# Kernel tuning notes

Hardware: AMD Instinct MI355X
Metric: run time of the kernel (lower is better)

The kernel has to match this reference:

```python
import jax, jax.numpy as jnp
import numpy as np

N_NODES = 100000
N_EDGES = 3200000
D_FEAT = 256
TOP_K = 50000


def setup_inputs() -> dict:
    key = jax.random.key(0)
    k1, k2, k3 = jax.random.split(key, 3)
    h = jax.random.normal(k1, (N_NODES, D_FEAT), dtype=jnp.float32)
    W = jax.random.normal(k2, (D_FEAT, 1), dtype=jnp.float32) * (1.0 / np.sqrt(D_FEAT))
    b = jnp.zeros((1,), dtype=jnp.float32)
    edge_index = jax.random.randint(k3, (2, N_EDGES), 0, N_NODES, dtype=jnp.int64)
    return {"h": h, "W": W, "b": b, "edge_index": edge_index, "top_k": TOP_K}


def reference(h, W, b, edge_index, top_k):
    # scores = sigmoid(Linear(h)) -> [N, 1]
    scores = jax.nn.sigmoid(h @ W + b)  # [N, 1]
    # top-k node selection by score (descending), like dgl.topk_nodes
    top_scores, node_ids = jax.lax.top_k(scores[:, 0], top_k)  # [k], [k]
    # gather features of selected nodes, scale by their scores
    new_h = h[node_ids] * top_scores[:, None]  # [k, d]
    # induced-subgraph edges: edge kept iff both endpoints selected
    member = jnp.zeros((h.shape[0],), dtype=bool).at[node_ids].set(True)
    edge_mask = member[edge_index[0]] & member[edge_index[1]]  # [E]
    return new_h, node_ids, edge_mask
```

## Files before the change

### kernel.cpp

```cpp
#include <hip/hip_runtime.h>
#include <math.h>

#define N_NODES 100000
#define D_FEAT  256
#define TOP_K   50000
#define NBINS   65536
#define NCHUNK  64
#define CUTPOS  (N_NODES - TOP_K)
#define ROWSTRIDE 260
#define NBITW   3200
#define FUSE_GRID   2048
#define EMIT_BLOCKS 1408


__device__ __forceinline__ int bucket_of(float s) {
    int b = (int)(s * 65536.0f);
    return min(max(b, 0), NBINS - 1);
}

__device__ __forceinline__ float np_expf(float x) {
    float q  = rintf(x * 1.44269504088896341f);
    float xr = fmaf(-q, 0.693359375f, x);
    xr       = fmaf(-q, -2.12194440e-4f, xr);
    float x2 = xr * xr;
    float p  = 1.9875691500E-4f;
    p = fmaf(p, xr, 1.3981999507E-3f);
    p = fmaf(p, xr, 8.3334519073E-3f);
    p = fmaf(p, xr, 4.1665795894E-2f);
    p = fmaf(p, xr, 1.6666665459E-1f);
    p = fmaf(p, xr, 5.0000001201E-1f);
    p = fmaf(p, x2, xr);
    p = p + 1.0f;
    return ldexpf(p, (int)q);
}

__global__ void score_kernel(const float* __restrict__ h,
                             const float* __restrict__ W,
                             const float* __restrict__ bvec,
                             float* __restrict__ s32,
                             int* __restrict__ hist) {
    __shared__ float rows[32 * ROWSTRIDE];
    __shared__ float wl[256];
    int tid  = threadIdx.x;
    int wave = tid >> 6;
    int lane = tid & 63;
    int g    = lane >> 3;
    int l    = lane & 7;

    wl[tid] = W[tid];

    int nodeBase = blockIdx.x * 32 + wave * 8;
#pragma unroll
    for (int r = 0; r < 8; ++r) {
        float4 v = ((const float4*)(h + (size_t)(nodeBase + r) * D_FEAT))[lane];
        *((float4*)&rows[(wave * 8 + r) * ROWSTRIDE + lane * 4]) = v;
    }
    __syncthreads();

    float wreg[32];
#pragma unroll
    for (int i = 0; i < 32; ++i) wreg[i] = wl[i * 8 + l];

    const float* myrow = &rows[(wave * 8 + g) * ROWSTRIDE];
    float acc = 0.0f;
#pragma unroll
    for (int i = 0; i < 32; ++i)
        acc = fmaf(myrow[i * 8 + l], wreg[i], acc);

    float b01 = acc + __shfl_xor(acc, 1, 64);
    float b23 = b01 + __shfl_xor(b01, 2, 64);
    float z   = b23 + __shfl_xor(b23, 4, 64);

    z = z + bvec[0];
    float t = np_expf(-z);
    float s = 1.0f / (1.0f + t);

    if (l == 0) {
        int node = nodeBase + g;
        s32[node] = s;
        atomicAdd(&hist[bucket_of(s)], 1);
    }
}

__global__ void scan_chunks_kernel(const int* __restrict__ hist,
                                   int* __restrict__ offs,
                                   int* __restrict__ cursor,
                                   int* __restrict__ chunkSum) {
    __shared__ int wsum[4];
    int tid  = threadIdx.x;
    int lane = tid & 63;
    int wid  = tid >> 6;
    int base = blockIdx.x * 1024 + tid * 4;

    int4 hv = *((const int4*)(hist + base));
    int e1 = hv.x;
    int e2 = hv.x + hv.y;
    int e3 = e2 + hv.z;
    int tot = e3 + hv.w;

    int incl = tot;
#pragma unroll
    for (int d = 1; d < 64; d <<= 1) {
        int t = __shfl_up(incl, d, 64);
        if (lane >= d) incl += t;
    }
    if (lane == 63) wsum[wid] = incl;
    __syncthreads();
    int wbase = 0;
#pragma unroll
    for (int w = 0; w < 3; ++w)
        if (w < wid) wbase += wsum[w];

    int excl = wbase + (incl - tot);
    int4 ov = make_int4(excl, excl + e1, excl + e2, excl + e3);
    *((int4*)(offs + base))   = ov;
    *((int4*)(cursor + base)) = ov;
    if (tid == 255) chunkSum[blockIdx.x] = excl + tot;
}

__device__ __forceinline__ void build_base(const int* __restrict__ chunkSum,
                                           int* sbase, int tid) {
    if (tid < 64) {
        int v = chunkSum[tid];
        int inc = v;
#pragma unroll
        for (int d = 1; d < 64; d <<= 1) {
            int t = __shfl_up(inc, d, 64);
            if (tid >= d) inc += t;
        }
        sbase[tid] = inc - v;
    }
}

__global__ void scatter_kernel(const float* __restrict__ s32,
                               int* __restrict__ cursor,
                               const int* __restrict__ offs,
                               const int* __restrict__ chunkSum,
                               unsigned int* __restrict__ bits,
                               float* __restrict__ ss,
                               int* __restrict__ si) {
    __shared__ int sbase[64];
    int tid = threadIdx.x;
    build_base(chunkSum, sbase, tid);
    __syncthreads();
    int i = blockIdx.x * 256 + tid;
    if (i >= N_NODES) return;
    float s = s32[i];
    int b = bucket_of(s);
    int bn = b + 1;
    int gend = (bn == NBINS) ? N_NODES : sbase[bn >> 10] + offs[bn];
    if (gend <= CUTPOS) return;
    int pos = atomicAdd(&cursor[b], 1);
    int gbase = sbase[b >> 10];
    ss[gbase + pos] = s;
    si[gbase + pos] = i;
    if (gbase + offs[b] >= CUTPOS)
        atomicOr(&bits[(unsigned)i >> 5], 1u << (i & 31));
}

__global__ void bucket_sort_kernel(const int* __restrict__ offs,
                                   const int* __restrict__ chunkSum,
                                   unsigned int* __restrict__ bits,
                                   float* __restrict__ ss,
                                   int* __restrict__ si) {
    __shared__ int sbase[64];
    int tid = threadIdx.x;
    build_base(chunkSum, sbase, tid);
    __syncthreads();
    int b = blockIdx.x * 256 + tid;
    int s0 = sbase[b >> 10] + offs[b];
    int e  = (b == NBINS - 1) ? N_NODES : sbase[(b + 1) >> 10] + offs[b + 1];
    if (e <= CUTPOS) return;
    for (int i = s0 + 1; i < e; ++i) {
        float ks = ss[i];
        int   ki = si[i];
        int j = i - 1;
        while (j >= s0) {
            float ps = ss[j];
            int   pi = si[j];
            bool gt = (ps > ks) || (ps == ks && pi < ki);
            if (!gt) break;
            ss[j + 1] = ps;
            si[j + 1] = pi;
            --j;
        }
        ss[j + 1] = ks;
        si[j + 1] = ki;
    }
    if (s0 < CUTPOS) {
        for (int i = CUTPOS; i < e; ++i) {
            int id = si[i];
            atomicOr(&bits[(unsigned)id >> 5], 1u << (id & 31));
        }
    }
}

__device__ __forceinline__ unsigned mem_bit(const unsigned int* __restrict__ bits,
                                            int s) {
    return (bits[(unsigned)s >> 5] >> (s & 31)) & 1u;
}

__global__ void emit_edge_kernel(const float* __restrict__ h,
                                 const float* __restrict__ ss,
                                 const int* __restrict__ si,
                                 const int* __restrict__ ei,
                                 const unsigned int* __restrict__ bits,
                                 float* __restrict__ out_newh,
                                 float* __restrict__ out_ids,
                                 float* __restrict__ out_mask,
                                 int E) {
    int tid = threadIdx.x;
    int bid = blockIdx.x;

    if (bid < EMIT_BLOCKS) {
        int lane = tid & 63;
        int wg   = bid * 4 + (tid >> 6);
        for (int row = wg; row < TOP_K; row += EMIT_BLOCKS * 4) {
            int p = N_NODES - 1 - row;
            int id  = si[p];
            float s = ss[p];
            if (lane == 0) out_ids[row] = (float)id;
            const float4* hv = (const float4*)(h + (size_t)id * D_FEAT);
            float4 v = hv[lane];
            ((float4*)(out_newh + (size_t)row * D_FEAT))[lane] =
                make_float4(v.x * s, v.y * s, v.z * s, v.w * s);
        }
        return;
    }

    __shared__ int sflag;
    if (tid < 64) {
        int v = ei[2 * tid + 1];
        unsigned long long m = __ballot(v == 0);
        if (tid == 0) sflag = (m == ~0ULL) ? 1 : 0;
    }
    __syncthreads();
    int flag = sflag;

    int npairs = (E + 1) / 2;
    int stride = (FUSE_GRID - EMIT_BLOCKS) * 256;
    for (int k = (bid - EMIT_BLOCKS) * 256 + tid; k < npairs; k += stride) {
        int i0 = 2 * k;
        int i1 = i0 + 1;
        if (i1 < E) {
            int s0, d0, s1, d1;
            if (flag) {
                int4 a  = ((const int4*)ei)[k];
                int4 bq = ((const int4*)(ei + 2 * (size_t)E))[k];
                s0 = a.x;  s1 = a.z;
                d0 = bq.x; d1 = bq.z;
            } else {
                int2 a  = ((const int2*)ei)[k];
                int2 bq = ((const int2*)(ei + (size_t)E))[k];
                s0 = a.x;  s1 = a.y;
                d0 = bq.x; d1 = bq.y;
            }
            bool ok0 = ((unsigned)s0 < (unsigned)N_NODES) &&
                       ((unsigned)d0 < (unsigned)N_NODES) &&
                       mem_bit(bits, s0) && mem_bit(bits, d0);
            bool ok1 = ((unsigned)s1 < (unsigned)N_NODES) &&
                       ((unsigned)d1 < (unsigned)N_NODES) &&
                       mem_bit(bits, s1) && mem_bit(bits, d1);
            ((float2*)out_mask)[k] = make_float2(ok0 ? 1.0f : 0.0f,
                                                 ok1 ? 1.0f : 0.0f);
        } else {
            int s0, d0;
            if (flag) { s0 = ei[2 * i0]; d0 = ei[2 * ((size_t)E + i0)]; }
            else      { s0 = ei[i0];     d0 = ei[(size_t)E + i0]; }
            bool ok0 = ((unsigned)s0 < (unsigned)N_NODES) &&
                       ((unsigned)d0 < (unsigned)N_NODES) &&
                       mem_bit(bits, s0) && mem_bit(bits, d0);
            out_mask[i0] = ok0 ? 1.0f : 0.0f;
        }
    }
}

extern "C" void kernel_launch(void* const* d_in, const int* in_sizes, int n_in,
                              void* d_out, int out_size, void* d_ws, size_t ws_size,
                              hipStream_t stream) {
    const float* h  = (const float*)d_in[0];
    const float* W  = (const float*)d_in[1];
    const float* bv = (const float*)d_in[2];
    const int*   ei = (const int*)d_in[3];
    const int E = in_sizes[3] / 2;

    char* ws = (char*)d_ws;
    float*        s32      = (float*)(ws + 0);
    float*        ss       = (float*)(ws + 400000);
    int*          si       = (int*)(ws + 800000);
    int*          hist     = (int*)(ws + 1200000);
    unsigned int* bits     = (unsigned int*)(ws + 1462144);
    int*          offs     = (int*)(ws + 1562144);
    int*          cursor   = (int*)(ws + 1824288);
    int*          chunkSum = (int*)(ws + 2086432);

    float* out      = (float*)d_out;
    float* out_newh = out;
    float* out_ids  = out + (size_t)TOP_K * D_FEAT;
    float* out_mask = out + (size_t)TOP_K * D_FEAT + TOP_K;

    hipMemsetAsync(ws + 1200000, 0, 274944, stream);

    score_kernel<<<N_NODES / 32, 256, 0, stream>>>(h, W, bv, s32, hist);
    scan_chunks_kernel<<<NCHUNK, 256, 0, stream>>>(hist, offs, cursor, chunkSum);
    scatter_kernel<<<(N_NODES + 255) / 256, 256, 0, stream>>>(s32, cursor, offs,
                                                              chunkSum, bits, ss, si);
    bucket_sort_kernel<<<NBINS / 256, 256, 0, stream>>>(offs, chunkSum, bits, ss, si);
    emit_edge_kernel<<<FUSE_GRID, 256, 0, stream>>>(h, ss, si, ei, bits,
                                                    out_newh, out_ids, out_mask, E);
}
```

Baseline: 238.7 us.

## Replace static block split with atomic work queue interleaving gather and edge chunks

The fused emit/edge kernel used to split blocks statically, with 1408 blocks doing row gathers and the rest doing edge-mask work. Now every block pulls chunks from a global atomic counter, and gather and edge chunks are interleaved 2:1 when the sizes match. Each gather chunk covers 8 rows and each edge chunk 512 pairs. The aim is to balance load between the two memory-bound phases and avoid tail imbalance, at the cost of one atomic plus two barriers per chunk and a slightly larger memset for the queue counter.

```diff
diff --git a/kernel.cpp b/kernel.cpp
--- a/kernel.cpp
+++ b/kernel.cpp
@@ -9,8 +9,9 @@
 #define CUTPOS  (N_NODES - TOP_K)
 #define ROWSTRIDE 260
 #define NBITW   3200
-#define FUSE_GRID   2048
-#define EMIT_BLOCKS 1408
+#define QGRID   2048
+#define EMIT_CHUNKS 6250
+#define EDGE_CHUNK_SHIFT 9
 
 
 __device__ __forceinline__ int bucket_of(float s) {
@@ -205,73 +206,104 @@
                                  const int* __restrict__ si,
                                  const int* __restrict__ ei,
                                  const unsigned int* __restrict__ bits,
+                                 int* __restrict__ queue,
                                  float* __restrict__ out_newh,
                                  float* __restrict__ out_ids,
                                  float* __restrict__ out_mask,
                                  int E) {
-    int tid = threadIdx.x;
-    int bid = blockIdx.x;
-
-    if (bid < EMIT_BLOCKS) {
-        int lane = tid & 63;
-        int wg   = bid * 4 + (tid >> 6);
-        for (int row = wg; row < TOP_K; row += EMIT_BLOCKS * 4) {
-            int p = N_NODES - 1 - row;
-            int id  = si[p];
-            float s = ss[p];
-            if (lane == 0) out_ids[row] = (float)id;
-            const float4* hv = (const float4*)(h + (size_t)id * D_FEAT);
-            float4 v = hv[lane];
-            ((float4*)(out_newh + (size_t)row * D_FEAT))[lane] =
-                make_float4(v.x * s, v.y * s, v.z * s, v.w * s);
-        }
-        return;
-    }
-
     __shared__ int sflag;
+    __shared__ int snext;
+    int tid  = threadIdx.x;
+    int lane = tid & 63;
+    int wv   = tid >> 6;
+
     if (tid < 64) {
         int v = ei[2 * tid + 1];
         unsigned long long m = __ballot(v == 0);
         if (tid == 0) sflag = (m == ~0ULL) ? 1 : 0;
     }
+
+    int npairs = (E + 1) / 2;
+    int nEdgeChunks = (npairs + ((1 << EDGE_CHUNK_SHIFT) - 1)) >> EDGE_CHUNK_SHIFT;
+    int total = EMIT_CHUNKS + nEdgeChunks;
+    bool interleave = (nEdgeChunks * 2 == EMIT_CHUNKS);
+
+    if (tid == 0) snext = atomicAdd(queue, 1);
     __syncthreads();
     int flag = sflag;
-
-    int npairs = (E + 1) / 2;
-    int stride = (FUSE_GRID - EMIT_BLOCKS) * 256;
-    for (int k = (bid - EMIT_BLOCKS) * 256 + tid; k < npairs; k += stride) {
-        int i0 = 2 * k;
-        int i1 = i0 + 1;
-        if (i1 < E) {
-            int s0, d0, s1, d1;
-            if (flag) {
-                int4 a  = ((const int4*)ei)[k];
-                int4 bq = ((const int4*)(ei + 2 * (size_t)E))[k];
-                s0 = a.x;  s1 = a.z;
-                d0 = bq.x; d1 = bq.z;
-            } else {
-                int2 a  = ((const int2*)ei)[k];
-                int2 bq = ((const int2*)(ei + (size_t)E))[k];
-                s0 = a.x;  s1 = a.y;
-                d0 = bq.x; d1 = bq.y;
+    int c = snext;
+
+    while (c < total) {
+        int grabbed = 0;
+        if (tid == 0) grabbed = atomicAdd(queue, 1);
+
+        int eIdx = -1, gIdx = -1;
+        if (interleave) {
+            int t = c / 3, r = c - 3 * t;
+            if (r < 2) eIdx = 2 * t + r; else gIdx = t;
+        } else {
+            if (c < EMIT_CHUNKS) eIdx = c; else gIdx = c - EMIT_CHUNKS;
+        }
+
+        if (eIdx >= 0) {
+            int rowBase = eIdx * 8 + wv * 2;
+#pragma unroll
+            for (int r = 0; r < 2; ++r) {
+                int row = rowBase + r;
+                int p = N_NODES - 1 - row;
+                int id  = si[p];
+                float s = ss[p];
+                if (lane == 0) out_ids[row] = (float)id;
+                const float4* hv = (const float4*)(h + (size_t)id * D_FEAT);
+                float4 v = hv[lane];
+                ((float4*)(out_newh + (size_t)row * D_FEAT))[lane] =
+                    make_float4(v.x * s, v.y * s, v.z * s, v.w * s);
             }
-            bool ok0 = ((unsigned)s0 < (unsigned)N_NODES) &&
-                       ((unsigned)d0 < (unsigned)N_NODES) &&
-                       mem_bit(bits, s0) && mem_bit(bits, d0);
-            bool ok1 = ((unsigned)s1 < (unsigned)N_NODES) &&
-                       ((unsigned)d1 < (unsigned)N_NODES) &&
-                       mem_bit(bits, s1) && mem_bit(bits, d1);
-            ((float2*)out_mask)[k] = make_float2(ok0 ? 1.0f : 0.0f,
-                                                 ok1 ? 1.0f : 0.0f);
         } else {
-            int s0, d0;
-            if (flag) { s0 = ei[2 * i0]; d0 = ei[2 * ((size_t)E + i0)]; }
-            else      { s0 = ei[i0];     d0 = ei[(size_t)E + i0]; }
-            bool ok0 = ((unsigned)s0 < (unsigned)N_NODES) &&
-                       ((unsigned)d0 < (unsigned)N_NODES) &&
-                       mem_bit(bits, s0) && mem_bit(bits, d0);
-            out_mask[i0] = ok0 ? 1.0f : 0.0f;
-        }
+            int base = gIdx << EDGE_CHUNK_SHIFT;
+#pragma unroll
+            for (int j = 0; j < 2; ++j) {
+                int k = base + j * 256 + tid;
+                if (k >= npairs) break;
+                int i0 = 2 * k;
+                int i1 = i0 + 1;
+                if (i1 < E) {
+                    int s0, d0, s1, d1;
+                    if (flag) {
+                        int4 a  = ((const int4*)ei)[k];
+                        int4 bq = ((const int4*)(ei + 2 * (size_t)E))[k];
+                        s0 = a.x;  s1 = a.z;
+                        d0 = bq.x; d1 = bq.z;
+                    } else {
+                        int2 a  = ((const int2*)ei)[k];
+                        int2 bq = ((const int2*)(ei + (size_t)E))[k];
+                        s0 = a.x;  s1 = a.y;
+                        d0 = bq.x; d1 = bq.y;
+                    }
+                    bool ok0 = ((unsigned)s0 < (unsigned)N_NODES) &&
+                               ((unsigned)d0 < (unsigned)N_NODES) &&
+                               mem_bit(bits, s0) && mem_bit(bits, d0);
+                    bool ok1 = ((unsigned)s1 < (unsigned)N_NODES) &&
+                               ((unsigned)d1 < (unsigned)N_NODES) &&
+                               mem_bit(bits, s1) && mem_bit(bits, d1);
+                    ((float2*)out_mask)[k] = make_float2(ok0 ? 1.0f : 0.0f,
+                                                         ok1 ? 1.0f : 0.0f);
+                } else {
+                    int s0, d0;
+                    if (flag) { s0 = ei[2 * i0]; d0 = ei[2 * ((size_t)E + i0)]; }
+                    else      { s0 = ei[i0];     d0 = ei[(size_t)E + i0]; }
+                    bool ok0 = ((unsigned)s0 < (unsigned)N_NODES) &&
+                               ((unsigned)d0 < (unsigned)N_NODES) &&
+                               mem_bit(bits, s0) && mem_bit(bits, d0);
+                    out_mask[i0] = ok0 ? 1.0f : 0.0f;
+                }
+            }
+        }
+
+        if (tid == 0) snext = grabbed;
+        __syncthreads();
+        c = snext;
+        __syncthreads();
     }
 }
 
@@ -290,6 +322,7 @@
     int*          si       = (int*)(ws + 800000);
     int*          hist     = (int*)(ws + 1200000);
     unsigned int* bits     = (unsigned int*)(ws + 1462144);
+    int*          queue    = (int*)(ws + 1474944);
     int*          offs     = (int*)(ws + 1562144);
     int*          cursor   = (int*)(ws + 1824288);
     int*          chunkSum = (int*)(ws + 2086432);
@@ -299,13 +332,13 @@
     float* out_ids  = out + (size_t)TOP_K * D_FEAT;
     float* out_mask = out + (size_t)TOP_K * D_FEAT + TOP_K;
 
-    hipMemsetAsync(ws + 1200000, 0, 274944, stream);
+    hipMemsetAsync(ws + 1200000, 0, 275008, stream);
 
     score_kernel<<<N_NODES / 32, 256, 0, stream>>>(h, W, bv, s32, hist);
     scan_chunks_kernel<<<NCHUNK, 256, 0, stream>>>(hist, offs, cursor, chunkSum);
     scatter_kernel<<<(N_NODES + 255) / 256, 256, 0, stream>>>(s32, cursor, offs,
                                                               chunkSum, bits, ss, si);
     bucket_sort_kernel<<<NBINS / 256, 256, 0, stream>>>(offs, chunkSum, bits, ss, si);
-    emit_edge_kernel<<<FUSE_GRID, 256, 0, stream>>>(h, ss, si, ei, bits,
-                                                    out_newh, out_ids, out_mask, E);
-}
+    emit_edge_kernel<<<QGRID, 256, 0, stream>>>(h, ss, si, ei, bits, queue,
+                                                out_newh, out_ids, out_mask, E);
+}
```

Result: slower. 336.4 us (+41.0%).
